# Performance work log

Measured on AMD Instinct MI355X. Metric: run time of the kernel, lower is better.

## Reference

```python
import jax, jax.numpy as jnp
import numpy as np

DIM_V = 512
NUM_HEADS = 8
LN_EPS = 1e-5


def _layernorm(x):
    # LayerNorm over last dim, no affine (simplified_layer_norm=True)
    mu = jnp.mean(x, axis=-1, keepdims=True)
    var = jnp.mean(jnp.square(x - mu), axis=-1, keepdims=True)
    return (x - mu) * jax.lax.rsqrt(var + LN_EPS)


def setup_inputs() -> dict:
    key = jax.random.key(0)
    ks = jax.random.split(key, 12)
    B, Nq, Nk, dQ, dK, dV = 16, 1024, 1024, 512, 512, DIM_V
    s = 0.02
    return {
        "Q": jax.random.normal(ks[0], (B, Nq, dQ), jnp.float32),
        "K": jax.random.normal(ks[1], (B, Nk, dK), jnp.float32),
        "Wq": jax.random.normal(ks[2], (dQ, dV), jnp.float32) * s,
        "bq": jnp.zeros((dV,), jnp.float32),
        "Wk": jax.random.normal(ks[3], (dK, dV), jnp.float32) * s,
        "bk": jnp.zeros((dV,), jnp.float32),
        "Wv": jax.random.normal(ks[4], (dK, dV), jnp.float32) * s,
        "bv": jnp.zeros((dV,), jnp.float32),
        "Wo": jax.random.normal(ks[5], (dV, dV), jnp.float32) * s,
        "bo": jnp.zeros((dV,), jnp.float32),
    }


def reference(Q, K, Wq, bq, Wk, bk, Wv, bv, Wo, bo):
    H = NUM_HEADS
    dh = DIM_V // H
    q = Q @ Wq + bq            # [B, Nq, dV]
    k = K @ Wk + bk            # [B, Nk, dV]
    v = K @ Wv + bv            # [B, Nk, dV]
    B, Nq, _ = q.shape
    Nk = k.shape[1]
    qh = q.reshape(B, Nq, H, dh)
    kh = k.reshape(B, Nk, H, dh)
    vh = v.reshape(B, Nk, H, dh)
    # NOTE: faithful to source — scale by sqrt(dim_V), not sqrt(head_dim)
    scores = jnp.einsum('bqhd,bkhd->bhqk', qh, kh) / jnp.sqrt(jnp.asarray(DIM_V, q.dtype))
    A = jax.nn.softmax(scores, axis=-1)                    # [B, H, Nq, Nk]
    attn = jnp.einsum('bhqk,bkhd->bqhd', A, vh).reshape(B, Nq, DIM_V)
    O = q + attn               # residual with projected Q
    O = _layernorm(O)          # ln0 (no affine)
    O = O + jax.nn.gelu(O @ Wo + bo, approximate=False)
    O = _layernorm(O)          # ln1 (no affine)
    return O
```

## Files before the change

### kernel.cpp

```cpp
#include <hip/hip_runtime.h>
#include <hip/hip_bf16.h>
#include <math.h>

typedef __bf16 bf16;
typedef __bf16 bf16x8 __attribute__((ext_vector_type(8)));
typedef float  f32x4  __attribute__((ext_vector_type(4)));
typedef float  f32x16 __attribute__((ext_vector_type(16)));
typedef unsigned u32x4 __attribute__((ext_vector_type(4)));

#define MFMA16(a,b,c) __builtin_amdgcn_mfma_f32_16x16x32_bf16((a),(b),(c),0,0,0)
#define MFMA32(a,b,c) __builtin_amdgcn_mfma_f32_32x32x16_bf16((a),(b),(c),0,0,0)
#define ATT_SCALE 0.0441941738241592f

__device__ __forceinline__ void async16p(const void* g, void* l) {
    __builtin_amdgcn_global_load_lds((const __attribute__((address_space(1))) void*)g,
                                     (__attribute__((address_space(3))) void*)l,
                                     16, 0, 0);
}

__device__ __forceinline__ unsigned pkbf(float a, float b) {
    union { bf16 h[2]; unsigned u; } x;
    x.h[0] = (bf16)a; x.h[1] = (bf16)b; return x.u;
}

__device__ __forceinline__ void plswap(unsigned &a, unsigned &b) {
#if __has_builtin(__builtin_amdgcn_permlane32_swap)
    auto r = __builtin_amdgcn_permlane32_swap((int)a, (int)b, false, false);
    a = (unsigned)r[0]; b = (unsigned)r[1];
#else
    unsigned sa = (unsigned)__shfl_xor((int)a, 32);
    unsigned sb = (unsigned)__shfl_xor((int)b, 32);
    bool hi = (threadIdx.x & 32) != 0;
    unsigned na = hi ? sb : a;
    unsigned nb = hi ? b  : sa;
    a = na; b = nb;
#endif
}

__global__ __launch_bounds__(256) void prep_w_kernel(
    const float* __restrict__ Wq, const float* __restrict__ Wk,
    const float* __restrict__ Wv, const float* __restrict__ Wo,
    bf16* __restrict__ WqT, bf16* __restrict__ WkT,
    bf16* __restrict__ WvT, bf16* __restrict__ WoT)
{
    __shared__ float tile[32][33];
    const int bx = blockIdx.x;
    const float* W; bf16* T;
    switch (bx >> 8) {
      case 0: W=Wq; T=WqT; break;
      case 1: W=Wk; T=WkT; break;
      case 2: W=Wv; T=WvT; break;
      default: W=Wo; T=WoT; break;
    }
    const int rest = bx & 255;
    const int k0 = (rest & 15) * 32, n0 = (rest >> 4) * 32;
    const int tx = threadIdx.x & 31, ty = threadIdx.x >> 5;
    #pragma unroll
    for (int i=0;i<32;i+=8)
        tile[ty+i][tx] = W[(size_t)(k0+ty+i)*512 + n0+tx];
    __syncthreads();
    #pragma unroll
    for (int i=0;i<32;i+=8)
        T[(size_t)(n0+ty+i)*512 + k0+tx] = (bf16)tile[tx][ty+i];
}

__global__ __launch_bounds__(256, 3) void gemm_qkv_kernel(
    const float* __restrict__ Qf, const float* __restrict__ Kf,
    const bf16* __restrict__ WqT, const bf16* __restrict__ WkT,
    const bf16* __restrict__ WvT,
    const float* __restrict__ bq, const float* __restrict__ bk,
    const float* __restrict__ bv,
    bf16* __restrict__ qbb, bf16* __restrict__ kbb, bf16* __restrict__ vT)
{
    __shared__ __align__(16) char smem[49152];
    float* As32 = (float*)smem;
    bf16*  Bs   = (bf16*)(smem + 32768);
    bf16*  Lt   = (bf16*)smem;

    const int z = blockIdx.z;
    const float* A  = (z == 0) ? Qf  : Kf;
    const bf16*  BT = (z == 0) ? WqT : (z == 1) ? WkT : WvT;
    const float* bb = (z == 0) ? bq  : (z == 1) ? bk  : bv;

    const int m0 = blockIdx.x * 128, n0 = blockIdx.y * 128;
    const int tid = threadIdx.x;
    const int lane = tid & 63, wave = tid >> 6;
    const int qd = lane >> 4, lr = lane & 15;
    const int wm = (wave & 1) * 64, wn = (wave >> 1) * 64;

    const float* gA = A + (size_t)(m0 + (tid>>3))*512 + (((tid&7)^((tid>>3)&7))*4);
    const bf16*  gB = BT + (size_t)(n0 + (tid>>2))*512 + (((tid&3)^((tid>>3)&3))*8);

    f32x4 acc[4][4];
    #pragma unroll
    for (int i=0;i<4;i++)
      #pragma unroll
      for (int j=0;j<4;j++) acc[i][j] = (f32x4){0,0,0,0};

    auto stage = [&](int buf, int k0) {
        float* lA = As32 + buf*4096 + wave*256;
        bf16*  lB = Bs   + buf*4096 + wave*512;
        #pragma unroll
        for (int i=0;i<4;i++)
            async16p(gA + k0 + (size_t)i*32*512, lA + i*1024);
        async16p(gB + k0,                  lB);
        async16p(gB + k0 + (size_t)64*512, lB + 2048);
    };

    stage(0, 0);
    for (int t = 0; t < 16; ++t) {
        const int cur = t & 1;
        __builtin_amdgcn_sched_barrier(0);
        __builtin_amdgcn_s_barrier();
        if (t < 15) {
            stage(cur ^ 1, (t+1)*32);
            asm volatile("s_waitcnt vmcnt(6)" ::: "memory");
        } else {
            asm volatile("s_waitcnt vmcnt(0)" ::: "memory");
        }
        __builtin_amdgcn_s_barrier();

        const float* Ab = As32 + cur*4096;
        const bf16*  Bb = Bs   + cur*4096;
        bf16x8 af[4], bfr[4];
        #pragma unroll
        for (int mi=0;mi<4;mi++) {
            int row = wm + mi*16 + lr;
            f32x4 f0 = *(f32x4*)(Ab + row*32 + (((qd*2  )^(lr&7))*4));
            f32x4 f1 = *(f32x4*)(Ab + row*32 + (((qd*2+1)^(lr&7))*4));
            bf16x8 a;
            a[0]=(bf16)f0[0]; a[1]=(bf16)f0[1]; a[2]=(bf16)f0[2]; a[3]=(bf16)f0[3];
            a[4]=(bf16)f1[0]; a[5]=(bf16)f1[1]; a[6]=(bf16)f1[2]; a[7]=(bf16)f1[3];
            af[mi] = a;
        }
        #pragma unroll
        for (int ni=0;ni<4;ni++)
            bfr[ni] = *(bf16x8*)(Bb + (wn+ni*16+lr)*32 + ((qd^((lr>>1)&3))*8));
        #pragma unroll
        for (int mi=0;mi<4;mi++)
          #pragma unroll
          for (int ni=0;ni<4;ni++)
            acc[mi][ni] = MFMA16(af[mi], bfr[ni], acc[mi][ni]);
    }

    if (z < 2) {
        bf16* C = (z == 0) ? qbb : kbb;
        #pragma unroll
        for (int ni=0;ni<4;ni++) {
            int n = n0 + wn + ni*16 + lr;
            float bv0 = bb[n];
            #pragma unroll
            for (int mi=0;mi<4;mi++) {
                int mb = m0 + wm + mi*16 + qd*4;
                #pragma unroll
                for (int r=0;r<4;r++)
                    C[(size_t)(mb+r)*512 + n] = (bf16)(acc[mi][ni][r] + bv0);
            }
        }
    } else {
        const int b = m0 >> 10, tok0 = m0 & 1023;
        const int row = tid >> 2, ch = tid & 3;
        #pragma unroll
        for (int half = 0; half < 2; ++half) {
            __syncthreads();
            if ((wn >> 6) == half) {
                #pragma unroll
                for (int ni=0;ni<4;ni++) {
                    int nl = ni*16 + lr;
                    float bvv = bb[n0 + half*64 + nl];
                    #pragma unroll
                    for (int mi=0;mi<4;mi++)
                      #pragma unroll
                      for (int r=0;r<4;r++) {
                        int col = wm + mi*16 + qd*4 + r;
                        Lt[nl*128 + ((((col>>3)^(nl&7))<<3) | (col&7))]
                            = (bf16)(acc[mi][ni][r] + bvv);
                      }
                }
            }
            __syncthreads();
            const int h = (n0 >> 6) + half;
            bf16* dst = vT + ((size_t)((b*8 + h)*64 + row))*1024 + tok0 + ch*32;
            #pragma unroll
            for (int s=0;s<4;s++) {
                int g = (ch*4 + s) ^ (row & 7);
                *(uint4*)(dst + s*8) = *(uint4*)(Lt + row*128 + g*8);
            }
        }
    }
}

__global__ __launch_bounds__(256, 4) void attn_kernel(
    const bf16* __restrict__ qb, const bf16* __restrict__ kb,
    const bf16* __restrict__ vT, bf16* __restrict__ attnb)
{
    const int x = blockIdx.x;
    const int qt = x >> 7, h = x & 7, b = (x & 127) >> 3;
    const int tid = threadIdx.x, lane = tid & 63, wave = tid >> 6;
    const int l = lane & 31, hi = lane >> 5;
    const int q0w = qt*128 + wave*32;

    __shared__ __align__(16) bf16 kv[2][2][4096];
    __shared__ float ls[4][32];

    bf16x8 aq[4];
    {
        const bf16* qrow = qb + ((size_t)(b*1024 + q0w + l))*512 + h*64 + hi*8;
        #pragma unroll
        for (int st=0; st<4; ++st) aq[st] = *(const bf16x8*)(qrow + st*16);
    }

    const int srow = lane >> 3;
    const int sg   = (lane & 7) ^ srow;
    const bf16* kg0 = kb + ((size_t)(b*1024 + wave*8 + srow))*512 + h*64 + sg*8;
    const bf16* vg0 = vT + ((size_t)((b*8 + h)*64 + wave*8 + srow))*1024 + sg*8;

    auto stage = [&](int buf, int t) {
        const size_t ko = (size_t)t*64*512;
        async16p(kg0 + ko,                   &kv[buf][0][wave*512]);
        async16p(kg0 + ko + (size_t)32*512,  &kv[buf][0][2048 + wave*512]);
        async16p(vg0 + t*64,                 &kv[buf][1][wave*512]);
        async16p(vg0 + t*64 + 32*1024,       &kv[buf][1][2048 + wave*512]);
    };

    f32x16 accO[2];
    accO[0] = (f32x16)0.f; accO[1] = (f32x16)0.f;
    float lsum = 0.f;

    stage(0, 0);
    for (int t=0; t<16; ++t) {
        const int cur = t & 1;
        __builtin_amdgcn_sched_barrier(0);
        __builtin_amdgcn_s_barrier();
        if (t < 15) {
            stage(cur ^ 1, t + 1);
            asm volatile("s_waitcnt vmcnt(4)" ::: "memory");
        } else {
            asm volatile("s_waitcnt vmcnt(0)" ::: "memory");
        }
        __builtin_amdgcn_s_barrier();

        const bf16* Ks = kv[cur][0];
        const bf16* Vs = kv[cur][1];

        u32x4 paf[4];
        #pragma unroll
        for (int kb2=0; kb2<2; ++kb2) {
            f32x16 sT = (f32x16)0.f;
            #pragma unroll
            for (int st=0; st<4; ++st) {
                bf16x8 kf = *(const bf16x8*)(Ks + (kb2*32 + l)*64
                                               + (((st*2 + hi) ^ (l & 7))*8));
                sT = MFMA32(kf, aq[st], sT);
            }
            unsigned u[8];
            #pragma unroll
            for (int m=0; m<8; ++m) {
                float e0 = __expf(sT[2*m]   * ATT_SCALE);
                float e1 = __expf(sT[2*m+1] * ATT_SCALE);
                lsum += e0 + e1;
                u[m] = pkbf(e0, e1);
            }
            #pragma unroll
            for (int sb=0; sb<2; ++sb) {
                unsigned a0=u[4*sb], a1=u[4*sb+1], a2=u[4*sb+2], a3=u[4*sb+3];
                plswap(a0, a2);
                plswap(a1, a3);
                paf[kb2*2 + sb] = (u32x4){a0, a1, a2, a3};
            }
        }
        #pragma unroll
        for (int db=0; db<2; ++db) {
            f32x16 a = accO[db];
            #pragma unroll
            for (int st=0; st<4; ++st) {
                bf16x8 vf = *(const bf16x8*)(Vs + (db*32 + l)*64
                                               + (((st*2 + hi) ^ (l & 7))*8));
                u32x4 pp = paf[st];
                bf16x8 pf = *(bf16x8*)&pp;
                a = MFMA32(pf, vf, a);
            }
            accO[db] = a;
        }
    }

    lsum += __shfl_xor(lsum, 32);
    ls[wave][l] = lsum;
    __syncthreads();

    #pragma unroll
    for (int g=0; g<4; ++g) {
        f32x4 lv = *(const f32x4*)(&ls[wave][g*8 + hi*4]);
        f32x4 inv;
        #pragma unroll
        for (int i=0;i<4;i++) inv[i] = 1.f / lv[i];
        #pragma unroll
        for (int db=0; db<2; ++db) {
            #pragma unroll
            for (int i=0;i<4;i++) {
                int r = g*4 + i;
                int qrow = q0w + g*8 + hi*4 + i;
                size_t idx = ((size_t)(b*1024 + qrow))*512 + h*64 + db*32 + l;
                float o = accO[db][r] * inv[i] + (float)qb[idx];
                attnb[idx] = (bf16)o;
            }
        }
    }
}

__global__ __launch_bounds__(256) void ln0_kernel(
    const bf16* __restrict__ attnb, bf16* __restrict__ Obf)
{
    const int wave = threadIdx.x >> 6, lane = threadIdx.x & 63;
    const int row = blockIdx.x*4 + wave;
    const size_t base = (size_t)row*512 + lane*8;
    bf16x8 av = *(const bf16x8*)(attnb + base);
    float x[8];
    #pragma unroll
    for (int i=0;i<8;i++) x[i] = (float)av[i];
    float s1 = 0.f, s2 = 0.f;
    #pragma unroll
    for (int i=0;i<8;i++){ s1 += x[i]; s2 += x[i]*x[i]; }
    #pragma unroll
    for (int off=1; off<64; off<<=1) { s1 += __shfl_xor(s1, off); s2 += __shfl_xor(s2, off); }
    float mu  = s1 * (1.f/512.f);
    float var = s2 * (1.f/512.f) - mu*mu;
    float rstd = rsqrtf(var + 1e-5f);
    bf16x8 ob;
    #pragma unroll
    for (int i=0;i<8;i++) ob[i] = (bf16)((x[i]-mu)*rstd);
    *(bf16x8*)(Obf + base) = ob;
}

__device__ __forceinline__ void gemm_core(
    const bf16* __restrict__ A, const bf16* __restrict__ BT,
    int m0, int n0, char* smem, f32x4 (&acc)[4][4])
{
    bf16* As = (bf16*)smem;
    bf16* Bs = (bf16*)(smem + 16384);
    const int tid = threadIdx.x;
    const int lane = tid & 63, wave = tid >> 6;
    const int qd = lane >> 4, lr = lane & 15;
    const int wm = (wave & 1) * 64, wn = (wave >> 1) * 64;

    const int srow = tid >> 2;
    const int sgr  = ((tid & 3) ^ ((tid >> 3) & 3)) * 8;
    const bf16* gA = A  + (size_t)(m0 + srow)*512 + sgr;
    const bf16* gB = BT + (size_t)(n0 + srow)*512 + sgr;

    auto stage = [&](int buf, int k0) {
        bf16* lA = As + buf*4096 + wave*512;
        bf16* lB = Bs + buf*4096 + wave*512;
        async16p(gA + k0,                  lA);
        async16p(gA + k0 + (size_t)64*512, lA + 2048);
        async16p(gB + k0,                  lB);
        async16p(gB + k0 + (size_t)64*512, lB + 2048);
    };

    stage(0, 0);
    for (int t = 0; t < 16; ++t) {
        const int cur = t & 1;
        __builtin_amdgcn_sched_barrier(0);
        __builtin_amdgcn_s_barrier();
        if (t < 15) {
            stage(cur ^ 1, (t+1)*32);
            asm volatile("s_waitcnt vmcnt(4)" ::: "memory");
        } else {
            asm volatile("s_waitcnt vmcnt(0)" ::: "memory");
        }
        __builtin_amdgcn_s_barrier();

        const bf16* Ab = As + cur*4096;
        const bf16* Bb = Bs + cur*4096;
        bf16x8 af[4], bfr[4];
        #pragma unroll
        for (int mi=0;mi<4;mi++)
            af[mi] = *(bf16x8*)(Ab + (wm+mi*16+lr)*32 + ((qd^((lr>>1)&3))*8));
        #pragma unroll
        for (int ni=0;ni<4;ni++)
            bfr[ni] = *(bf16x8*)(Bb + (wn+ni*16+lr)*32 + ((qd^((lr>>1)&3))*8));
        #pragma unroll
        for (int mi=0;mi<4;mi++)
          #pragma unroll
          for (int ni=0;ni<4;ni++)
            acc[mi][ni] = MFMA16(af[mi], bfr[ni], acc[mi][ni]);
    }
}

__global__ __launch_bounds__(256, 4) void gemm_o_kernel(
    const bf16* __restrict__ Obf, const bf16* __restrict__ WoT,
    const float* __restrict__ bo, bf16* __restrict__ xb)
{
    __shared__ __align__(16) char smem[32768];
    const int m0 = blockIdx.x * 128, n0 = blockIdx.y * 128;
    const int tid = threadIdx.x;
    const int lane = tid & 63, wave = tid >> 6;
    const int qd = lane >> 4, lr = lane & 15;
    const int wm = (wave & 1) * 64, wn = (wave >> 1) * 64;

    f32x4 acc[4][4];
    #pragma unroll
    for (int i=0;i<4;i++)
      #pragma unroll
      for (int j=0;j<4;j++) acc[i][j] = (f32x4){0,0,0,0};

    gemm_core(Obf, WoT, m0, n0, smem, acc);

    #pragma unroll
    for (int ni=0;ni<4;ni++) {
        int n = n0 + wn + ni*16 + lr;
        float bv = bo[n];
        #pragma unroll
        for (int mi=0;mi<4;mi++) {
            int mb = m0 + wm + mi*16 + qd*4;
            #pragma unroll
            for (int r=0;r<4;r++) {
                float g = acc[mi][ni][r] + bv;
                float gelu = 0.5f * g * (1.f + erff(g * 0.70710678118654752f));
                size_t idx = (size_t)(mb+r)*512 + n;
                xb[idx] = (bf16)((float)Obf[idx] + gelu);
            }
        }
    }
}

__global__ __launch_bounds__(256) void ln1_kernel(
    const bf16* __restrict__ xb, float* __restrict__ out)
{
    const int wave = threadIdx.x >> 6, lane = threadIdx.x & 63;
    const int row = blockIdx.x*4 + wave;
    const size_t base = (size_t)row*512 + lane*8;
    bf16x8 xv = *(const bf16x8*)(xb + base);
    float x[8];
    #pragma unroll
    for (int i=0;i<8;i++) x[i] = (float)xv[i];
    float s1 = 0.f, s2 = 0.f;
    #pragma unroll
    for (int i=0;i<8;i++){ s1 += x[i]; s2 += x[i]*x[i]; }
    #pragma unroll
    for (int off=1; off<64; off<<=1) { s1 += __shfl_xor(s1, off); s2 += __shfl_xor(s2, off); }
    float mu  = s1 * (1.f/512.f);
    float var = s2 * (1.f/512.f) - mu*mu;
    float rstd = rsqrtf(var + 1e-5f);
    float4 o0 = {(x[0]-mu)*rstd,(x[1]-mu)*rstd,(x[2]-mu)*rstd,(x[3]-mu)*rstd};
    float4 o1 = {(x[4]-mu)*rstd,(x[5]-mu)*rstd,(x[6]-mu)*rstd,(x[7]-mu)*rstd};
    *(float4*)(out + base)     = o0;
    *(float4*)(out + base + 4) = o1;
}

extern "C" void kernel_launch(void* const* d_in, const int* in_sizes, int n_in,
                              void* d_out, int out_size, void* d_ws, size_t ws_size,
                              hipStream_t stream)
{
    (void)in_sizes; (void)n_in; (void)out_size; (void)ws_size;
    const float* Q  = (const float*)d_in[0];
    const float* K  = (const float*)d_in[1];
    const float* Wq = (const float*)d_in[2];
    const float* bq = (const float*)d_in[3];
    const float* Wk = (const float*)d_in[4];
    const float* bk = (const float*)d_in[5];
    const float* Wv = (const float*)d_in[6];
    const float* bv = (const float*)d_in[7];
    const float* Wo = (const float*)d_in[8];
    const float* bo = (const float*)d_in[9];
    float* out = (float*)d_out;

    const size_t nTok = (size_t)16*1024*512;
    char* p = (char*)d_ws;
    auto alloc = [&](size_t bytes)->char* {
        char* r = p; p += (bytes + 255) & ~(size_t)255; return r;
    };
    bf16* WqT   = (bf16*)alloc(512*512*2);
    bf16* WkT   = (bf16*)alloc(512*512*2);
    bf16* WvT   = (bf16*)alloc(512*512*2);
    bf16* WoT   = (bf16*)alloc(512*512*2);
    bf16* qbb   = (bf16*)alloc(nTok*2);
    bf16* kbb   = (bf16*)alloc(nTok*2);
    bf16* vT    = (bf16*)alloc(nTok*2);
    bf16* attnb = (bf16*)alloc(nTok*2);
    bf16* Obf   = (bf16*)alloc(nTok*2);
    bf16* xb    = (bf16*)alloc(nTok*2);

    prep_w_kernel<<<1024, 256, 0, stream>>>(Wq, Wk, Wv, Wo, WqT, WkT, WvT, WoT);
    gemm_qkv_kernel<<<dim3(128,4,3), 256, 0, stream>>>(Q, K, WqT, WkT, WvT,
                                                       bq, bk, bv, qbb, kbb, vT);
    attn_kernel<<<dim3(1024), 256, 0, stream>>>(qbb, kbb, vT, attnb);
    ln0_kernel<<<4096, 256, 0, stream>>>(attnb, Obf);
    gemm_o_kernel<<<dim3(128,4), 256, 0, stream>>>(Obf, WoT, bo, xb);
    ln1_kernel<<<4096, 256, 0, stream>>>(xb, out);
}
```

Measured before the change: 257.4 us.

## Share A tiles across K/V and Q projections, fold scale into K, retile O GEMM

Each projection block now computes two 128-wide output tiles from one staged A tile: K and V together for the K input, and two column halves for Q. This halves how often the fp32 activations are loaded and converted. The softmax scale (times log2 e) is folded into K so the attention loop can use a raw exp2. The attention kernel also gets a new LDS swizzle and s_setprio hints around its MFMA sections. The output GEMM moves to 64-row tiles with more blocks. The costs are doubled accumulator registers and lower occupancy in the projection kernel, plus K rounded to bf16 after scaling.

```diff
diff --git a/kernel.cpp b/kernel.cpp
--- a/kernel.cpp
+++ b/kernel.cpp
@@ -10,12 +10,20 @@
 
 #define MFMA16(a,b,c) __builtin_amdgcn_mfma_f32_16x16x32_bf16((a),(b),(c),0,0,0)
 #define MFMA32(a,b,c) __builtin_amdgcn_mfma_f32_32x32x16_bf16((a),(b),(c),0,0,0)
-#define ATT_SCALE 0.0441941738241592f
+#define KSCALE 0.0637587159f
 
 __device__ __forceinline__ void async16p(const void* g, void* l) {
     __builtin_amdgcn_global_load_lds((const __attribute__((address_space(1))) void*)g,
                                      (__attribute__((address_space(3))) void*)l,
                                      16, 0, 0);
+}
+
+__device__ __forceinline__ float fexp2(float x) {
+#if __has_builtin(__builtin_amdgcn_exp2f)
+    return __builtin_amdgcn_exp2f(x);
+#else
+    return exp2f(x);
+#endif
 }
 
 __device__ __forceinline__ unsigned pkbf(float a, float b) {
@@ -64,7 +72,7 @@
         T[(size_t)(n0+ty+i)*512 + k0+tx] = (bf16)tile[tx][ty+i];
 }
 
-__global__ __launch_bounds__(256, 3) void gemm_qkv_kernel(
+__global__ __launch_bounds__(256, 2) void gemm_proj_kernel(
     const float* __restrict__ Qf, const float* __restrict__ Kf,
     const bf16* __restrict__ WqT, const bf16* __restrict__ WkT,
     const bf16* __restrict__ WvT,
@@ -72,39 +80,55 @@
     const float* __restrict__ bv,
     bf16* __restrict__ qbb, bf16* __restrict__ kbb, bf16* __restrict__ vT)
 {
-    __shared__ __align__(16) char smem[49152];
+    __shared__ __align__(16) char smem[65536];
     float* As32 = (float*)smem;
     bf16*  Bs   = (bf16*)(smem + 32768);
     bf16*  Lt   = (bf16*)smem;
 
-    const int z = blockIdx.z;
-    const float* A  = (z == 0) ? Qf  : Kf;
-    const bf16*  BT = (z == 0) ? WqT : (z == 1) ? WkT : WvT;
-    const float* bb = (z == 0) ? bq  : (z == 1) ? bk  : bv;
-
-    const int m0 = blockIdx.x * 128, n0 = blockIdx.y * 128;
+    const int x = blockIdx.x;
+    const bool isQ = (x < 256);
+    int m0, n0;
+    const float* A; const bf16 *BT0, *BT1; const float *bb0, *bb1;
+    if (isQ) {
+        m0 = (x >> 1) * 128; n0 = (x & 1) * 128;
+        A = Qf; BT0 = WqT + (size_t)n0*512; BT1 = WqT + (size_t)(n0+256)*512;
+        bb0 = bq + n0; bb1 = bq + n0 + 256;
+    } else {
+        int r = x - 256;
+        m0 = (r >> 2) * 128; n0 = (r & 3) * 128;
+        A = Kf; BT0 = WkT + (size_t)n0*512; BT1 = WvT + (size_t)n0*512;
+        bb0 = bk + n0; bb1 = bv + n0;
+    }
+
     const int tid = threadIdx.x;
     const int lane = tid & 63, wave = tid >> 6;
     const int qd = lane >> 4, lr = lane & 15;
     const int wm = (wave & 1) * 64, wn = (wave >> 1) * 64;
 
     const float* gA = A + (size_t)(m0 + (tid>>3))*512 + (((tid&7)^((tid>>3)&7))*4);
-    const bf16*  gB = BT + (size_t)(n0 + (tid>>2))*512 + (((tid&3)^((tid>>3)&3))*8);
-
-    f32x4 acc[4][4];
-    #pragma unroll
-    for (int i=0;i<4;i++)
+    const int bgr = ((tid & 3) ^ ((tid >> 3) & 3)) * 8;
+    const bf16* gB0 = BT0 + (size_t)(tid>>2)*512 + bgr;
+    const bf16* gB1 = BT1 + (size_t)(tid>>2)*512 + bgr;
+
+    f32x4 acc[2][4][4];
+    #pragma unroll
+    for (int p=0;p<2;p++)
       #pragma unroll
-      for (int j=0;j<4;j++) acc[i][j] = (f32x4){0,0,0,0};
+      for (int i=0;i<4;i++)
+        #pragma unroll
+        for (int j=0;j<4;j++) acc[p][i][j] = (f32x4){0,0,0,0};
 
     auto stage = [&](int buf, int k0) {
         float* lA = As32 + buf*4096 + wave*256;
-        bf16*  lB = Bs   + buf*4096 + wave*512;
         #pragma unroll
         for (int i=0;i<4;i++)
             async16p(gA + k0 + (size_t)i*32*512, lA + i*1024);
-        async16p(gB + k0,                  lB);
-        async16p(gB + k0 + (size_t)64*512, lB + 2048);
+        bf16* lB0 = Bs + buf*8192 + wave*512;
+        async16p(gB0 + k0,                  lB0);
+        async16p(gB0 + k0 + (size_t)64*512, lB0 + 2048);
+        bf16* lB1 = Bs + buf*8192 + 4096 + wave*512;
+        async16p(gB1 + k0,                  lB1);
+        async16p(gB1 + k0 + (size_t)64*512, lB1 + 2048);
     };
 
     stage(0, 0);
@@ -114,15 +138,15 @@
         __builtin_amdgcn_s_barrier();
         if (t < 15) {
             stage(cur ^ 1, (t+1)*32);
-            asm volatile("s_waitcnt vmcnt(6)" ::: "memory");
+            asm volatile("s_waitcnt vmcnt(8)" ::: "memory");
         } else {
             asm volatile("s_waitcnt vmcnt(0)" ::: "memory");
         }
         __builtin_amdgcn_s_barrier();
 
         const float* Ab = As32 + cur*4096;
-        const bf16*  Bb = Bs   + cur*4096;
-        bf16x8 af[4], bfr[4];
+        const bf16*  Bb = Bs   + cur*8192;
+        bf16x8 af[4], bfr[2][4];
         #pragma unroll
         for (int mi=0;mi<4;mi++) {
             int row = wm + mi*16 + lr;
@@ -134,30 +158,52 @@
             af[mi] = a;
         }
         #pragma unroll
-        for (int ni=0;ni<4;ni++)
-            bfr[ni] = *(bf16x8*)(Bb + (wn+ni*16+lr)*32 + ((qd^((lr>>1)&3))*8));
-        #pragma unroll
-        for (int mi=0;mi<4;mi++)
+        for (int p=0;p<2;p++)
           #pragma unroll
           for (int ni=0;ni<4;ni++)
-            acc[mi][ni] = MFMA16(af[mi], bfr[ni], acc[mi][ni]);
-    }
-
-    if (z < 2) {
-        bf16* C = (z == 0) ? qbb : kbb;
+            bfr[p][ni] = *(bf16x8*)(Bb + p*4096 + (wn+ni*16+lr)*32
+                                       + ((qd^((lr>>1)&3))*8));
+        #pragma unroll
+        for (int p=0;p<2;p++)
+          #pragma unroll
+          for (int mi=0;mi<4;mi++)
+            #pragma unroll
+            for (int ni=0;ni<4;ni++)
+              acc[p][mi][ni] = MFMA16(af[mi], bfr[p][ni], acc[p][mi][ni]);
+    }
+
+    if (isQ) {
+        #pragma unroll
+        for (int p=0;p<2;p++) {
+            const float* bb = p ? bb1 : bb0;
+            #pragma unroll
+            for (int ni=0;ni<4;ni++) {
+                int nl = wn + ni*16 + lr;
+                int n = n0 + p*256 + nl;
+                float bv0 = bb[nl];
+                #pragma unroll
+                for (int mi=0;mi<4;mi++) {
+                    int mb = m0 + wm + mi*16 + qd*4;
+                    #pragma unroll
+                    for (int r=0;r<4;r++)
+                        qbb[(size_t)(mb+r)*512 + n] = (bf16)(acc[p][mi][ni][r] + bv0);
+                }
+            }
+        }
+    } else {
         #pragma unroll
         for (int ni=0;ni<4;ni++) {
-            int n = n0 + wn + ni*16 + lr;
-            float bv0 = bb[n];
+            int nl = wn + ni*16 + lr;
+            int n = n0 + nl;
+            float bv0 = bb0[nl];
             #pragma unroll
             for (int mi=0;mi<4;mi++) {
                 int mb = m0 + wm + mi*16 + qd*4;
                 #pragma unroll
                 for (int r=0;r<4;r++)
-                    C[(size_t)(mb+r)*512 + n] = (bf16)(acc[mi][ni][r] + bv0);
-            }
-        }
-    } else {
+                    kbb[(size_t)(mb+r)*512 + n] = (bf16)((acc[0][mi][ni][r] + bv0)*KSCALE);
+            }
+        }
         const int b = m0 >> 10, tok0 = m0 & 1023;
         const int row = tid >> 2, ch = tid & 3;
         #pragma unroll
@@ -167,14 +213,14 @@
                 #pragma unroll
                 for (int ni=0;ni<4;ni++) {
                     int nl = ni*16 + lr;
-                    float bvv = bb[n0 + half*64 + nl];
+                    float bvv = bb1[half*64 + nl];
                     #pragma unroll
                     for (int mi=0;mi<4;mi++)
                       #pragma unroll
                       for (int r=0;r<4;r++) {
                         int col = wm + mi*16 + qd*4 + r;
                         Lt[nl*128 + ((((col>>3)^(nl&7))<<3) | (col&7))]
-                            = (bf16)(acc[mi][ni][r] + bvv);
+                            = (bf16)(acc[1][mi][ni][r] + bvv);
                       }
                 }
             }
@@ -211,21 +257,25 @@
     }
 
     const int srow = lane >> 3;
-    const int sg   = (lane & 7) ^ srow;
-    const bf16* kg0 = kb + ((size_t)(b*1024 + wave*8 + srow))*512 + h*64 + sg*8;
-    const bf16* vg0 = vT + ((size_t)((b*8 + h)*64 + wave*8 + srow))*1024 + sg*8;
+    const int sgA  = (lane & 7) ^ srow ^ wave;
+    const int sgB  = sgA ^ 4;
+    const bf16* kg0 = kb + ((size_t)(b*1024 + wave*8 + srow))*512      + h*64 + sgA*8;
+    const bf16* kg1 = kb + ((size_t)(b*1024 + wave*8 + srow + 32))*512 + h*64 + sgB*8;
+    const bf16* vg0 = vT + ((size_t)((b*8 + h)*64 + wave*8 + srow))*1024      + sgA*8;
+    const bf16* vg1 = vT + ((size_t)((b*8 + h)*64 + wave*8 + srow + 32))*1024 + sgB*8;
 
     auto stage = [&](int buf, int t) {
         const size_t ko = (size_t)t*64*512;
-        async16p(kg0 + ko,                   &kv[buf][0][wave*512]);
-        async16p(kg0 + ko + (size_t)32*512,  &kv[buf][0][2048 + wave*512]);
-        async16p(vg0 + t*64,                 &kv[buf][1][wave*512]);
-        async16p(vg0 + t*64 + 32*1024,       &kv[buf][1][2048 + wave*512]);
+        async16p(kg0 + ko,     &kv[buf][0][wave*512]);
+        async16p(kg1 + ko,     &kv[buf][0][2048 + wave*512]);
+        async16p(vg0 + t*64,   &kv[buf][1][wave*512]);
+        async16p(vg1 + t*64,   &kv[buf][1][2048 + wave*512]);
     };
 
     f32x16 accO[2];
     accO[0] = (f32x16)0.f; accO[1] = (f32x16)0.f;
     float lsum = 0.f;
+    const int kx = (l & 7) ^ (l >> 3);
 
     stage(0, 0);
     for (int t=0; t<16; ++t) {
@@ -247,17 +297,19 @@
         #pragma unroll
         for (int kb2=0; kb2<2; ++kb2) {
             f32x16 sT = (f32x16)0.f;
+            __builtin_amdgcn_s_setprio(1);
             #pragma unroll
             for (int st=0; st<4; ++st) {
                 bf16x8 kf = *(const bf16x8*)(Ks + (kb2*32 + l)*64
-                                               + (((st*2 + hi) ^ (l & 7))*8));
+                               + (((st*2 + hi) ^ kx ^ (kb2<<2))*8));
                 sT = MFMA32(kf, aq[st], sT);
             }
+            __builtin_amdgcn_s_setprio(0);
             unsigned u[8];
             #pragma unroll
             for (int m=0; m<8; ++m) {
-                float e0 = __expf(sT[2*m]   * ATT_SCALE);
-                float e1 = __expf(sT[2*m+1] * ATT_SCALE);
+                float e0 = fexp2(sT[2*m]);
+                float e1 = fexp2(sT[2*m+1]);
                 lsum += e0 + e1;
                 u[m] = pkbf(e0, e1);
             }
@@ -269,19 +321,21 @@
                 paf[kb2*2 + sb] = (u32x4){a0, a1, a2, a3};
             }
         }
+        __builtin_amdgcn_s_setprio(1);
         #pragma unroll
         for (int db=0; db<2; ++db) {
             f32x16 a = accO[db];
             #pragma unroll
             for (int st=0; st<4; ++st) {
                 bf16x8 vf = *(const bf16x8*)(Vs + (db*32 + l)*64
-                                               + (((st*2 + hi) ^ (l & 7))*8));
+                               + (((st*2 + hi) ^ kx ^ (db<<2))*8));
                 u32x4 pp = paf[st];
                 bf16x8 pf = *(bf16x8*)&pp;
                 a = MFMA32(pf, vf, a);
             }
             accO[db] = a;
         }
+        __builtin_amdgcn_s_setprio(0);
     }
 
     lsum += __shfl_xor(lsum, 32);
@@ -332,27 +386,32 @@
     *(bf16x8*)(Obf + base) = ob;
 }
 
-__device__ __forceinline__ void gemm_core(
-    const bf16* __restrict__ A, const bf16* __restrict__ BT,
-    int m0, int n0, char* smem, f32x4 (&acc)[4][4])
-{
+__global__ __launch_bounds__(256, 4) void gemm_o_kernel(
+    const bf16* __restrict__ Obf, const bf16* __restrict__ WoT,
+    const float* __restrict__ bo, bf16* __restrict__ xb)
+{
+    __shared__ __align__(16) char smem[24576];
     bf16* As = (bf16*)smem;
-    bf16* Bs = (bf16*)(smem + 16384);
+    bf16* Bs = (bf16*)(smem + 8192);
+    const int m0 = blockIdx.x * 64, n0 = blockIdx.y * 128;
     const int tid = threadIdx.x;
     const int lane = tid & 63, wave = tid >> 6;
     const int qd = lane >> 4, lr = lane & 15;
-    const int wm = (wave & 1) * 64, wn = (wave >> 1) * 64;
-
-    const int srow = tid >> 2;
-    const int sgr  = ((tid & 3) ^ ((tid >> 3) & 3)) * 8;
-    const bf16* gA = A  + (size_t)(m0 + srow)*512 + sgr;
-    const bf16* gB = BT + (size_t)(n0 + srow)*512 + sgr;
+    const int wm = (wave & 1) * 32, wn = (wave >> 1) * 64;
+
+    const int bgr = ((tid & 3) ^ ((tid >> 3) & 3)) * 8;
+    const bf16* gA = Obf + (size_t)(m0 + (tid>>2))*512 + bgr;
+    const bf16* gB = WoT + (size_t)(n0 + (tid>>2))*512 + bgr;
+
+    f32x4 acc[2][4];
+    #pragma unroll
+    for (int i=0;i<2;i++)
+      #pragma unroll
+      for (int j=0;j<4;j++) acc[i][j] = (f32x4){0,0,0,0};
 
     auto stage = [&](int buf, int k0) {
-        bf16* lA = As + buf*4096 + wave*512;
+        async16p(gA + k0,                  As + buf*2048 + wave*512);
         bf16* lB = Bs + buf*4096 + wave*512;
-        async16p(gA + k0,                  lA);
-        async16p(gA + k0 + (size_t)64*512, lA + 2048);
         async16p(gB + k0,                  lB);
         async16p(gB + k0 + (size_t)64*512, lB + 2048);
     };
@@ -364,54 +423,34 @@
         __builtin_amdgcn_s_barrier();
         if (t < 15) {
             stage(cur ^ 1, (t+1)*32);
-            asm volatile("s_waitcnt vmcnt(4)" ::: "memory");
+            asm volatile("s_waitcnt vmcnt(3)" ::: "memory");
         } else {
             asm volatile("s_waitcnt vmcnt(0)" ::: "memory");
         }
         __builtin_amdgcn_s_barrier();
 
-        const bf16* Ab = As + cur*4096;
+        const bf16* Ab = As + cur*2048;
         const bf16* Bb = Bs + cur*4096;
-        bf16x8 af[4], bfr[4];
-        #pragma unroll
-        for (int mi=0;mi<4;mi++)
+        bf16x8 af[2], bfr[4];
+        #pragma unroll
+        for (int mi=0;mi<2;mi++)
             af[mi] = *(bf16x8*)(Ab + (wm+mi*16+lr)*32 + ((qd^((lr>>1)&3))*8));
         #pragma unroll
         for (int ni=0;ni<4;ni++)
             bfr[ni] = *(bf16x8*)(Bb + (wn+ni*16+lr)*32 + ((qd^((lr>>1)&3))*8));
         #pragma unroll
-        for (int mi=0;mi<4;mi++)
+        for (int mi=0;mi<2;mi++)
           #pragma unroll
           for (int ni=0;ni<4;ni++)
             acc[mi][ni] = MFMA16(af[mi], bfr[ni], acc[mi][ni]);
     }
-}
-
-__global__ __launch_bounds__(256, 4) void gemm_o_kernel(
-    const bf16* __restrict__ Obf, const bf16* __restrict__ WoT,
-    const float* __restrict__ bo, bf16* __restrict__ xb)
-{
-    __shared__ __align__(16) char smem[32768];
-    const int m0 = blockIdx.x * 128, n0 = blockIdx.y * 128;
-    const int tid = threadIdx.x;
-    const int lane = tid & 63, wave = tid >> 6;
-    const int qd = lane >> 4, lr = lane & 15;
-    const int wm = (wave & 1) * 64, wn = (wave >> 1) * 64;
-
-    f32x4 acc[4][4];
-    #pragma unroll
-    for (int i=0;i<4;i++)
-      #pragma unroll
-      for (int j=0;j<4;j++) acc[i][j] = (f32x4){0,0,0,0};
-
-    gemm_core(Obf, WoT, m0, n0, smem, acc);
 
     #pragma unroll
     for (int ni=0;ni<4;ni++) {
         int n = n0 + wn + ni*16 + lr;
         float bv = bo[n];
         #pragma unroll
-        for (int mi=0;mi<4;mi++) {
+        for (int mi=0;mi<2;mi++) {
             int mb = m0 + wm + mi*16 + qd*4;
             #pragma unroll
             for (int r=0;r<4;r++) {
@@ -482,10 +521,10 @@
     bf16* xb    = (bf16*)alloc(nTok*2);
 
     prep_w_kernel<<<1024, 256, 0, stream>>>(Wq, Wk, Wv, Wo, WqT, WkT, WvT, WoT);
-    gemm_qkv_kernel<<<dim3(128,4,3), 256, 0, stream>>>(Q, K, WqT, WkT, WvT,
-                                                       bq, bk, bv, qbb, kbb, vT);
+    gemm_proj_kernel<<<768, 256, 0, stream>>>(Q, K, WqT, WkT, WvT,
+                                              bq, bk, bv, qbb, kbb, vT);
     attn_kernel<<<dim3(1024), 256, 0, stream>>>(qbb, kbb, vT, attnb);
     ln0_kernel<<<4096, 256, 0, stream>>>(attnb, Obf);
-    gemm_o_kernel<<<dim3(128,4), 256, 0, stream>>>(Obf, WoT, bo, xb);
+    gemm_o_kernel<<<dim3(256,4), 256, 0, stream>>>(Obf, WoT, bo, xb);
     ln1_kernel<<<4096, 256, 0, stream>>>(xb, out);
 }
```

Measured after the change: 251.5 us. -2.3%, faster.
